# Kernel optimization log

Hardware: AMD Instinct MI355X
Metric: run time of the kernel (lower is better)

## Reference

```python
import jax, jax.numpy as jnp
import numpy as np

D_MODEL = 1024
N_HEADS = 16
D_KEYS = 64
D_LLM = 4096
B, L, S = 8, 1024, 1000
HD = N_HEADS * D_KEYS  # 1024


def setup_inputs() -> dict:
    key = jax.random.key(0)
    ks = jax.random.split(key, 12)
    sd = lambda fan_in: 1.0 / np.sqrt(fan_in)
    return {
        "target_embedding": jax.random.normal(ks[0], (B, L, D_MODEL), jnp.float32),
        "source_embedding": jax.random.normal(ks[1], (S, D_LLM), jnp.float32),
        "value_embedding": jax.random.normal(ks[2], (S, D_LLM), jnp.float32),
        "Wq": jax.random.normal(ks[3], (D_MODEL, HD), jnp.float32) * sd(D_MODEL),
        "bq": jnp.zeros((HD,), jnp.float32),
        "Wk": jax.random.normal(ks[4], (D_LLM, HD), jnp.float32) * sd(D_LLM),
        "bk": jnp.zeros((HD,), jnp.float32),
        "Wv": jax.random.normal(ks[5], (D_LLM, HD), jnp.float32) * sd(D_LLM),
        "bv": jnp.zeros((HD,), jnp.float32),
        "Wo": jax.random.normal(ks[6], (HD, D_LLM), jnp.float32) * sd(HD),
        "bo": jnp.zeros((D_LLM,), jnp.float32),
        "alpha": jnp.asarray(1.0, jnp.float32),
        "beta": jnp.asarray(0.5, jnp.float32),
    }


def reference(target_embedding, source_embedding, value_embedding,
              Wq, bq, Wk, bk, Wv, bv, Wo, bo, alpha, beta):
    # Projections
    q = (target_embedding @ Wq + bq).reshape(B, L, N_HEADS, D_KEYS)   # blhe
    k = (source_embedding @ Wk + bk).reshape(S, N_HEADS, D_KEYS)      # she
    v = (value_embedding @ Wv + bv).reshape(S, N_HEADS, D_KEYS)       # she
    # Reprogramming attention with alpha/beta scaling
    scale = 1.0 / np.sqrt(D_KEYS)
    scores = jnp.einsum('blhe,she->bhls', alpha * q, beta * k)        # BxHxLxS
    A = jax.nn.softmax(scale * scores, axis=-1)  # dropout is identity in eval
    out = jnp.einsum('bhls,she->blhe', A, v)
    out = out.reshape(B, L, HD)
    return out @ Wo + bo                                              # B,L,d_llm
```

## Files before the change

### kernel.cpp

```cpp
#include <hip/hip_runtime.h>

typedef unsigned short u16;
typedef __attribute__((ext_vector_type(8))) short short8;
typedef __attribute__((ext_vector_type(4))) float floatx4;

#define LOG2E 1.4426950408889634f

__device__ __forceinline__ u16 f2bf(float f) {
    unsigned u = __builtin_bit_cast(unsigned, f);
    u += 0x7fffu + ((u >> 16) & 1u);
    return (u16)(u >> 16);
}

__device__ __forceinline__ void gl2lds16(const void* g, void* l) {
    __builtin_amdgcn_global_load_lds((const __attribute__((address_space(1))) void*)g,
                                     (__attribute__((address_space(3))) void*)l,
                                     16, 0, 0);
}

__global__ __launch_bounds__(256) void conv_all(const float* __restrict__ T, u16* __restrict__ Tb,
                                                const float* __restrict__ Se, u16* __restrict__ Seb,
                                                const float* __restrict__ Ve, u16* __restrict__ Veb) {
    int g = blockIdx.x * 256 + threadIdx.x;
    const float* s; u16* d; int i; int nsrc;
    if (g < 2097152)      { s = T;  d = Tb;  i = g * 4;               nsrc = 8388608; }
    else if (g < 3145728) { s = Se; d = Seb; i = (g - 2097152) * 4;   nsrc = 4096000; }
    else                  { s = Ve; d = Veb; i = (g - 3145728) * 4;   nsrc = 4096000; }
    ushort4 o;
    if (i < nsrc) {
        float4 v = *(const float4*)(s + i);
        o.x = f2bf(v.x); o.y = f2bf(v.y); o.z = f2bf(v.z); o.w = f2bf(v.w);
    } else {
        o = make_ushort4(0, 0, 0, 0);
    }
    *(ushort4*)(d + i) = o;
}

__device__ __forceinline__ void transpose_core(const float* __restrict__ W, u16* __restrict__ Wt,
                                               int Kd, int Nd, int kx, int ny) {
    __shared__ u16 t[64][65];
    const int tid = threadIdx.x;
    const int k0 = kx * 64, n0 = ny * 64;
#pragma unroll
    for (int i = 0; i < 16; i++) {
        int r = i * 4 + (tid >> 6), c = tid & 63;
        t[r][c] = f2bf(W[(size_t)(k0 + r) * Nd + n0 + c]);
    }
    __syncthreads();
#pragma unroll
    for (int i = 0; i < 16; i++) {
        int n = i * 4 + (tid >> 6), k = tid & 63;
        Wt[(size_t)(n0 + n) * Kd + k0 + k] = t[k][n];
    }
}

__global__ __launch_bounds__(256) void transpose3(const float* __restrict__ Wq, u16* __restrict__ WqT,
                                                  const float* __restrict__ Wk, u16* __restrict__ WkT,
                                                  const float* __restrict__ Wv, u16* __restrict__ WvT) {
    int id = blockIdx.x;
    if (id < 256)       transpose_core(Wq, WqT, 1024, 1024, id & 15, id >> 4);
    else if (id < 1280) { int t = id - 256;  transpose_core(Wk, WkT, 4096, 1024, t & 63, t >> 6); }
    else                { int t = id - 1280; transpose_core(Wv, WvT, 4096, 1024, t & 63, t >> 6); }
}


__device__ __forceinline__
void stage_half(u16* dstA, u16* dstB, const u16* gA, const u16* gB, int Ks, int wave, int lane) {
    int r = lane >> 2;
    int cp = (lane & 3) * 8;
    const u16* a0 = gA + (size_t)(wave * 32 + r) * Ks + cp;
    const u16* b0 = gB + (size_t)(wave * 32 + r) * Ks + cp;
    const u16* a1 = gA + (size_t)(wave * 32 + 16 + r) * Ks + cp;
    const u16* b1 = gB + (size_t)(wave * 32 + 16 + r) * Ks + cp;
    gl2lds16(a0, dstA + wave * 1024);
    gl2lds16(b0, dstB + wave * 1024);
    gl2lds16(a1, dstA + wave * 1024 + 512);
    gl2lds16(b1, dstB + wave * 1024 + 512);
}

__device__ __forceinline__
void gemm8_core(const u16* __restrict__ A, const u16* __restrict__ Bt,
                const float* __restrict__ bias, void* __restrict__ Cout,
                int M, int N, int Ks, int Klen, int koff,
                int mode, float mult, int m0, int n0, u16* lds) {
    const int tid = threadIdx.x;
    const int wave = tid >> 6, lane = tid & 63;
    const int quad = lane >> 4, l16 = lane & 15;
    const int wm = wave >> 2, wn = wave & 3;

    floatx4 acc[8][4];
#pragma unroll
    for (int i = 0; i < 8; i++)
#pragma unroll
        for (int j = 0; j < 4; j++) acc[i][j] = (floatx4){0.f, 0.f, 0.f, 0.f};

    const u16* Ag = A + (size_t)m0 * Ks + koff;
    const u16* Bg = Bt + (size_t)n0 * Ks + koff;
    const int NT = Klen >> 6;

    const int raw = (wm * 128 + l16) * 32 + quad * 8;
    const int rbw = (wn * 64 + l16) * 32 + quad * 8;

    stage_half(lds, lds + 16384, Ag, Bg, Ks, wave, lane);
    stage_half(lds + 8192, lds + 24576, Ag + 32, Bg + 32, Ks, wave, lane);

#pragma unroll 1
    for (int t = 0; t < NT; ++t) {
        u16* cur = lds + (t & 1) * 32768;
        u16* nxt = lds + ((t + 1) & 1) * 32768;
        const u16* An = Ag + (size_t)(t + 1) * 64;
        const u16* Bn = Bg + (size_t)(t + 1) * 64;
        const bool st = (t + 1 < NT);
        short8 af[4], bf[4];

        asm volatile("s_waitcnt vmcnt(4)" ::: "memory");
        __builtin_amdgcn_sched_barrier(0);
        __builtin_amdgcn_s_barrier();
#pragma unroll
        for (int i = 0; i < 4; i++) af[i] = *(const short8*)&cur[raw + i * 512];
#pragma unroll
        for (int j = 0; j < 4; j++) bf[j] = *(const short8*)&cur[16384 + rbw + j * 512];
        if (st) stage_half(nxt, nxt + 16384, An, Bn, Ks, wave, lane);
        __builtin_amdgcn_s_setprio(1);
#pragma unroll
        for (int i = 0; i < 4; i++)
#pragma unroll
            for (int j = 0; j < 4; j++)
                acc[i][j] = __builtin_amdgcn_mfma_f32_16x16x32_bf16(af[i], bf[j], acc[i][j], 0, 0, 0);
        __builtin_amdgcn_s_setprio(0);

        __builtin_amdgcn_s_barrier();
#pragma unroll
        for (int i = 0; i < 4; i++) af[i] = *(const short8*)&cur[raw + 2048 + i * 512];
        __builtin_amdgcn_s_setprio(1);
#pragma unroll
        for (int i = 0; i < 4; i++)
#pragma unroll
            for (int j = 0; j < 4; j++)
                acc[i + 4][j] = __builtin_amdgcn_mfma_f32_16x16x32_bf16(af[i], bf[j], acc[i + 4][j], 0, 0, 0);
        __builtin_amdgcn_s_setprio(0);

        if (st) { asm volatile("s_waitcnt vmcnt(4)" ::: "memory"); }
        else    { asm volatile("s_waitcnt vmcnt(0)" ::: "memory"); }
        __builtin_amdgcn_sched_barrier(0);
        __builtin_amdgcn_s_barrier();
#pragma unroll
        for (int i = 0; i < 4; i++) af[i] = *(const short8*)&cur[8192 + raw + i * 512];
#pragma unroll
        for (int j = 0; j < 4; j++) bf[j] = *(const short8*)&cur[24576 + rbw + j * 512];
        if (st) stage_half(nxt + 8192, nxt + 24576, An + 32, Bn + 32, Ks, wave, lane);
        __builtin_amdgcn_s_setprio(1);
#pragma unroll
        for (int i = 0; i < 4; i++)
#pragma unroll
            for (int j = 0; j < 4; j++)
                acc[i][j] = __builtin_amdgcn_mfma_f32_16x16x32_bf16(af[i], bf[j], acc[i][j], 0, 0, 0);
        __builtin_amdgcn_s_setprio(0);

        __builtin_amdgcn_s_barrier();
#pragma unroll
        for (int i = 0; i < 4; i++) af[i] = *(const short8*)&cur[8192 + raw + 2048 + i * 512];
        __builtin_amdgcn_s_setprio(1);
#pragma unroll
        for (int i = 0; i < 4; i++)
#pragma unroll
            for (int j = 0; j < 4; j++)
                acc[i + 4][j] = __builtin_amdgcn_mfma_f32_16x16x32_bf16(af[i], bf[j], acc[i + 4][j], 0, 0, 0);
        __builtin_amdgcn_s_setprio(0);
    }

#pragma unroll
    for (int i = 0; i < 8; i++) {
#pragma unroll
        for (int j = 0; j < 4; j++) {
            int col = n0 + wn * 64 + j * 16 + l16;
            float bvv = (mode >= 4) ? 0.0f : bias[col];
#pragma unroll
            for (int r = 0; r < 4; r++) {
                int row = m0 + wm * 128 + i * 16 + quad * 4 + r;
                float v = (acc[i][j][r] + bvv) * mult;
                if (mode == 3 || mode == 4) {
                    ((float*)Cout)[(size_t)row * N + col] = v;
                } else if (mode == 5) {
                    ((float*)Cout)[(size_t)col * M + row] = v;
                } else {
                    ((u16*)Cout)[(size_t)row * N + col] = f2bf(v);
                }
            }
        }
    }
}

__global__ __launch_bounds__(512, 2)
void gemm_qkv(const u16* __restrict__ Tb, const u16* __restrict__ WqT, const float* __restrict__ bq,
              const u16* __restrict__ Seb, const u16* __restrict__ WkT,
              const u16* __restrict__ Veb, const u16* __restrict__ WvT,
              u16* __restrict__ Qb, float* __restrict__ KP, float* __restrict__ VPT,
              const float* __restrict__ alphaP, const float* __restrict__ betaP) {
    __shared__ u16 lds[65536];
    int b0 = blockIdx.x;
    int w = (b0 & 7) * 32 + (b0 >> 3);
    if (w < 128) {
        float mult = alphaP[0] * betaP[0] * 0.125f * LOG2E;
        gemm8_core(Tb, WqT, bq, Qb, 8192, 1024, 1024, 1024, 0,
                   1, mult, (w >> 2) * 256, (w & 3) * 256, lds);
    } else if (w < 192) {
        int t = w - 128; int kc = t >> 4;
        gemm8_core(Seb, WkT, nullptr, KP + (size_t)kc * 1048576, 1024, 1024, 4096, 1024, kc * 1024,
                   4, 1.0f, ((t >> 2) & 3) * 256, (t & 3) * 256, lds);
    } else {
        int t = w - 192; int kc = t >> 4;
        gemm8_core(Veb, WvT, nullptr, VPT + (size_t)kc * 1048576, 1024, 1024, 4096, 1024, kc * 1024,
                   5, 1.0f, ((t >> 2) & 3) * 256, (t & 3) * 256, lds);
    }
}

__global__ __launch_bounds__(512, 2)
void gemm_final(const u16* __restrict__ A, const u16* __restrict__ Bt,
                const float* __restrict__ bias, float* __restrict__ Cout) {
    __shared__ u16 lds[65536];
    int b0 = blockIdx.x;
    int idx = b0 >> 3;
    int m = (b0 & 7) * 4 + (idx >> 4);
    int n = idx & 15;
    gemm8_core(A, Bt, bias, Cout, 8192, 4096, 1024, 1024, 0, 3, 1.0f, m * 256, n * 256, lds);
}

__global__ __launch_bounds__(256)
void reduce_wo(const float* __restrict__ KP, const float* __restrict__ bk, u16* __restrict__ Kb,
               const float* __restrict__ VPT, const float* __restrict__ bv, u16* __restrict__ VTb,
               const float* __restrict__ Wo, u16* __restrict__ WoT) {
    int id = blockIdx.x;
    if (id >= 2048) {
        int t = id - 2048;
        transpose_core(Wo, WoT, 1024, 4096, t & 15, t >> 4);
        return;
    }
    const int tid = threadIdx.x;
    if (id < 1024) {
        int r = id, c = tid * 4;
        size_t base = (size_t)r * 1024 + c;
        float4 a0 = *(const float4*)(KP + base);
        float4 a1 = *(const float4*)(KP + 1048576 + base);
        float4 a2 = *(const float4*)(KP + 2097152 + base);
        float4 a3 = *(const float4*)(KP + 3145728 + base);
        float4 bb = *(const float4*)(bk + c);
        ushort4 o;
        o.x = f2bf(a0.x + a1.x + a2.x + a3.x + bb.x);
        o.y = f2bf(a0.y + a1.y + a2.y + a3.y + bb.y);
        o.z = f2bf(a0.z + a1.z + a2.z + a3.z + bb.z);
        o.w = f2bf(a0.w + a1.w + a2.w + a3.w + bb.w);
        *(ushort4*)(Kb + base) = o;
    } else {
        int d = id - 1024, s = tid * 4;
        size_t base = (size_t)d * 1024 + s;
        float4 a0 = *(const float4*)(VPT + base);
        float4 a1 = *(const float4*)(VPT + 1048576 + base);
        float4 a2 = *(const float4*)(VPT + 2097152 + base);
        float4 a3 = *(const float4*)(VPT + 3145728 + base);
        float bvv = bv[d];
        ushort4 o;
        o.x = f2bf(a0.x + a1.x + a2.x + a3.x + bvv);
        o.y = f2bf(a0.y + a1.y + a2.y + a3.y + bvv);
        o.z = f2bf(a0.z + a1.z + a2.z + a3.z + bvv);
        o.w = f2bf(a0.w + a1.w + a2.w + a3.w + bvv);
        *(ushort4*)(VTb + base) = o;
    }
}

__global__ __launch_bounds__(256, 2)
void attn_kernel(const u16* __restrict__ Q, const u16* __restrict__ Kb,
                 const u16* __restrict__ VT, u16* __restrict__ O) {
    __shared__ u16 sK[128 * 64];
    __shared__ u16 sV[64 * 128];
    __shared__ u16 sP[128 * 128];
    const int tid = threadIdx.x;
    const int wave = tid >> 6, lane = tid & 63;
    const int quad = lane >> 4, l16 = lane & 15;
    const int l7 = l16 & 7;
    const int bid = blockIdx.x;
    const int qt = bid & 7, h = (bid >> 3) & 15, b = bid >> 7;

    const u16* Qbase = Q + ((size_t)(b * 1024 + qt * 128 + wave * 32)) * 1024 + h * 64;
    short8 qf[2][2];
#pragma unroll
    for (int i = 0; i < 2; i++)
#pragma unroll
        for (int kk = 0; kk < 2; kk++)
            qf[i][kk] = *(const short8*)&Qbase[(size_t)(i * 16 + l16) * 1024 + kk * 32 + quad * 8];

    float psum[2] = {0.f, 0.f};
    floatx4 oacc[2][4];
#pragma unroll
    for (int i = 0; i < 2; i++)
#pragma unroll
        for (int n = 0; n < 4; n++) oacc[i][n] = (floatx4){0.f, 0.f, 0.f, 0.f};

    for (int st = 0; st < 8; ++st) {
#pragma unroll
        for (int i = 0; i < 4; i++) {
            int r = i * 32 + wave * 8 + (lane >> 3);
            int c = ((lane & 7) ^ ((lane >> 3) & 7)) * 8;
            gl2lds16(Kb + (size_t)(st * 128 + r) * 1024 + h * 64 + c, sK + i * 2048 + wave * 512);
        }
#pragma unroll
        for (int i = 0; i < 4; i++) {
            int r = i * 16 + wave * 4 + (lane >> 4);
            int c = ((lane & 15) ^ ((wave * 4 + (lane >> 4)) & 7)) * 8;
            gl2lds16(VT + (size_t)(h * 64 + r) * 1024 + st * 128 + c, sV + i * 2048 + wave * 512);
        }
        __syncthreads();

        floatx4 sacc[2][8];
#pragma unroll
        for (int i = 0; i < 2; i++)
#pragma unroll
            for (int j = 0; j < 8; j++) sacc[i][j] = (floatx4){0.f, 0.f, 0.f, 0.f};
#pragma unroll
        for (int kk = 0; kk < 2; kk++) {
            short8 kf[8];
#pragma unroll
            for (int j = 0; j < 8; j++)
                kf[j] = *(const short8*)&sK[(j * 16 + l16) * 64 + (((kk * 4 + quad) ^ l7) * 8)];
#pragma unroll
            for (int i = 0; i < 2; i++)
#pragma unroll
                for (int j = 0; j < 8; j++)
                    sacc[i][j] = __builtin_amdgcn_mfma_f32_16x16x32_bf16(kf[j], qf[i][kk], sacc[i][j], 0, 0, 0);
        }

#pragma unroll
        for (int i = 0; i < 2; i++) {
            const int rowbase = (wave * 32 + i * 16 + l16) * 128;
#pragma unroll
            for (int j = 0; j < 8; j++) {
                float p0 = exp2f(sacc[i][j][0]);
                float p1 = exp2f(sacc[i][j][1]);
                float p2 = exp2f(sacc[i][j][2]);
                float p3 = exp2f(sacc[i][j][3]);
                if (st == 7) {
                    if (j == 7 || (j == 6 && quad >= 2)) { p0 = p1 = p2 = p3 = 0.f; }
                }
                psum[i] += (p0 + p1) + (p2 + p3);
                uint2 val;
                val.x = (unsigned)f2bf(p0) | ((unsigned)f2bf(p1) << 16);
                val.y = (unsigned)f2bf(p2) | ((unsigned)f2bf(p3) << 16);
                int chunk = (2 * j + (quad >> 1)) ^ l7;
                *(uint2*)&sP[rowbase + chunk * 8 + (quad & 1) * 4] = val;
            }
        }

#pragma unroll
        for (int c = 0; c < 4; c++) {
            short8 pf[2], vf[4];
#pragma unroll
            for (int i = 0; i < 2; i++)
                pf[i] = *(const short8*)&sP[(wave * 32 + i * 16 + l16) * 128 + (((c * 4 + quad) ^ l7) * 8)];
#pragma unroll
            for (int n = 0; n < 4; n++)
                vf[n] = *(const short8*)&sV[(n * 16 + l16) * 128 + (((c * 4 + quad) ^ l7) * 8)];
#pragma unroll
            for (int i = 0; i < 2; i++)
#pragma unroll
                for (int n = 0; n < 4; n++)
                    oacc[i][n] = __builtin_amdgcn_mfma_f32_16x16x32_bf16(pf[i], vf[n], oacc[i][n], 0, 0, 0);
        }
        __syncthreads();
    }

#pragma unroll
    for (int i = 0; i < 2; i++) {
        psum[i] += __shfl_xor(psum[i], 16);
        psum[i] += __shfl_xor(psum[i], 32);
    }

    u16* Obase = O + ((size_t)(b * 1024 + qt * 128 + wave * 32)) * 1024 + h * 64;
#pragma unroll
    for (int i = 0; i < 2; i++) {
#pragma unroll
        for (int r = 0; r < 4; r++) {
            float l = __shfl(psum[i], (lane & 48) | (quad * 4 + r));
            float linv = 1.0f / l;
#pragma unroll
            for (int n = 0; n < 4; n++)
                Obase[(size_t)(i * 16 + quad * 4 + r) * 1024 + n * 16 + l16] = f2bf(oacc[i][n][r] * linv);
        }
    }
}

extern "C" void kernel_launch(void* const* d_in, const int* in_sizes, int n_in,
                              void* d_out, int out_size, void* d_ws, size_t ws_size,
                              hipStream_t stream) {
    const float* T     = (const float*)d_in[0];
    const float* Se    = (const float*)d_in[1];
    const float* Ve    = (const float*)d_in[2];
    const float* Wq    = (const float*)d_in[3];
    const float* bq    = (const float*)d_in[4];
    const float* Wk    = (const float*)d_in[5];
    const float* bk    = (const float*)d_in[6];
    const float* Wv    = (const float*)d_in[7];
    const float* bv    = (const float*)d_in[8];
    const float* Wo    = (const float*)d_in[9];
    const float* bo    = (const float*)d_in[10];
    const float* alpha = (const float*)d_in[11];
    const float* beta  = (const float*)d_in[12];

    char* ws = (char*)d_ws;
    size_t off = 0;
    auto alloc = [&](size_t bytes) { size_t o = off; off += (bytes + 255) & ~(size_t)255; return o; };

    u16* Tb  = (u16*)(ws + alloc((size_t)8192 * 1024 * 2));
    u16* Seb = (u16*)(ws + alloc((size_t)1024 * 4096 * 2));
    u16* Veb = (u16*)(ws + alloc((size_t)1024 * 4096 * 2));
    u16* WqT = (u16*)(ws + alloc((size_t)1024 * 1024 * 2));
    u16* WkT = (u16*)(ws + alloc((size_t)1024 * 4096 * 2));
    u16* WvT = (u16*)(ws + alloc((size_t)1024 * 4096 * 2));
    u16* Qb  = (u16*)(ws + alloc((size_t)8192 * 1024 * 2));
    u16* Kb  = (u16*)(ws + alloc((size_t)1024 * 1024 * 2));
    u16* VTb = (u16*)(ws + alloc((size_t)1024 * 1024 * 2));
    float* KP  = (float*)(ws + alloc((size_t)4 * 1024 * 1024 * 4));
    float* VPT = (float*)(ws + alloc((size_t)4 * 1024 * 1024 * 4));
    u16* Ob  = Tb;
    u16* WoT = Veb;

    conv_all<<<16384, 256, 0, stream>>>(T, Tb, Se, Seb, Ve, Veb);
    transpose3<<<2304, 256, 0, stream>>>(Wq, WqT, Wk, WkT, Wv, WvT);
    gemm_qkv<<<256, 512, 0, stream>>>(Tb, WqT, bq, Seb, WkT, Veb, WvT,
                                      Qb, KP, VPT, alpha, beta);
    reduce_wo<<<3072, 256, 0, stream>>>(KP, bk, Kb, VPT, bv, VTb, Wo, WoT);
    attn_kernel<<<1024, 256, 0, stream>>>(Qb, Kb, VTb, Ob);
    gemm_final<<<512, 512, 0, stream>>>(Ob, WoT, bo, (float*)d_out);
}
```

Before: 433.1 us.

## Swizzle GEMM LDS tiles and restage full K-tiles with double buffering

The shared GEMM core now stores each 64-wide K tile as full 64-element rows with an XOR swizzle on the 16-byte column chunks, so fragment reads from shared memory hit fewer bank conflicts. Staging moves from two half-tiles per iteration to one full tile loaded two iterations ahead into the buffer just consumed, with a single wait and barrier per iteration. The aim is to cut LDS bank conflicts and barrier/waitcnt overhead in the projection GEMMs. It adds an extra barrier before restaging and relies on the swizzle staying consistent between the global-to-LDS copy and the fragment reads.

```diff
diff --git a/kernel.cpp b/kernel.cpp
--- a/kernel.cpp
+++ b/kernel.cpp
@@ -64,18 +64,19 @@
 }
 
 
+__device__ __forceinline__ short8 ldsfrag(const u16* b, int row, int kk, int quad, int l7) {
+    return *(const short8*)&b[row * 64 + (((kk * 4 + quad) ^ l7) * 8)];
+}
+
 __device__ __forceinline__
-void stage_half(u16* dstA, u16* dstB, const u16* gA, const u16* gB, int Ks, int wave, int lane) {
-    int r = lane >> 2;
-    int cp = (lane & 3) * 8;
-    const u16* a0 = gA + (size_t)(wave * 32 + r) * Ks + cp;
-    const u16* b0 = gB + (size_t)(wave * 32 + r) * Ks + cp;
-    const u16* a1 = gA + (size_t)(wave * 32 + 16 + r) * Ks + cp;
-    const u16* b1 = gB + (size_t)(wave * 32 + 16 + r) * Ks + cp;
-    gl2lds16(a0, dstA + wave * 1024);
-    gl2lds16(b0, dstB + wave * 1024);
-    gl2lds16(a1, dstA + wave * 1024 + 512);
-    gl2lds16(b1, dstB + wave * 1024 + 512);
+void stage_tile(u16* dA, u16* dB, const u16* gA, const u16* gB, int Ks, int wave, int lane) {
+    int rl = wave * 8 + (lane >> 3);
+    int cs = ((lane & 7) ^ (rl & 7)) * 8;
+#pragma unroll
+    for (int ii = 0; ii < 4; ii++) {
+        gl2lds16(gA + (size_t)(ii * 64 + rl) * Ks + cs, dA + ii * 4096 + wave * 512);
+        gl2lds16(gB + (size_t)(ii * 64 + rl) * Ks + cs, dB + ii * 4096 + wave * 512);
+    }
 }
 
 __device__ __forceinline__
@@ -85,7 +86,7 @@
                 int mode, float mult, int m0, int n0, u16* lds) {
     const int tid = threadIdx.x;
     const int wave = tid >> 6, lane = tid & 63;
-    const int quad = lane >> 4, l16 = lane & 15;
+    const int quad = lane >> 4, l16 = lane & 15, l7 = l16 & 7;
     const int wm = wave >> 2, wn = wave & 3;
 
     floatx4 acc[8][4];
@@ -98,29 +99,29 @@
     const u16* Bg = Bt + (size_t)n0 * Ks + koff;
     const int NT = Klen >> 6;
 
-    const int raw = (wm * 128 + l16) * 32 + quad * 8;
-    const int rbw = (wn * 64 + l16) * 32 + quad * 8;
-
-    stage_half(lds, lds + 16384, Ag, Bg, Ks, wave, lane);
-    stage_half(lds + 8192, lds + 24576, Ag + 32, Bg + 32, Ks, wave, lane);
+    const int ra = wm * 128 + l16;
+    const int rb = wn * 64 + l16;
+
+    u16* A0 = lds;          u16* B0 = lds + 16384;
+    u16* A1 = lds + 32768;  u16* B1 = lds + 49152;
+
+    stage_tile(A0, B0, Ag, Bg, Ks, wave, lane);
+    stage_tile(A1, B1, Ag + 64, Bg + 64, Ks, wave, lane);
+    asm volatile("s_waitcnt vmcnt(8)" ::: "memory");
+    __builtin_amdgcn_sched_barrier(0);
+    __builtin_amdgcn_s_barrier();
+    __builtin_amdgcn_sched_barrier(0);
 
 #pragma unroll 1
     for (int t = 0; t < NT; ++t) {
-        u16* cur = lds + (t & 1) * 32768;
-        u16* nxt = lds + ((t + 1) & 1) * 32768;
-        const u16* An = Ag + (size_t)(t + 1) * 64;
-        const u16* Bn = Bg + (size_t)(t + 1) * 64;
-        const bool st = (t + 1 < NT);
+        u16* cA = (t & 1) ? A1 : A0;
+        u16* cB = (t & 1) ? B1 : B0;
         short8 af[4], bf[4];
 
-        asm volatile("s_waitcnt vmcnt(4)" ::: "memory");
-        __builtin_amdgcn_sched_barrier(0);
-        __builtin_amdgcn_s_barrier();
-#pragma unroll
-        for (int i = 0; i < 4; i++) af[i] = *(const short8*)&cur[raw + i * 512];
-#pragma unroll
-        for (int j = 0; j < 4; j++) bf[j] = *(const short8*)&cur[16384 + rbw + j * 512];
-        if (st) stage_half(nxt, nxt + 16384, An, Bn, Ks, wave, lane);
+#pragma unroll
+        for (int i = 0; i < 4; i++) af[i] = ldsfrag(cA, ra + i * 16, 0, quad, l7);
+#pragma unroll
+        for (int j = 0; j < 4; j++) bf[j] = ldsfrag(cB, rb + j * 16, 0, quad, l7);
         __builtin_amdgcn_s_setprio(1);
 #pragma unroll
         for (int i = 0; i < 4; i++)
@@ -128,10 +129,10 @@
             for (int j = 0; j < 4; j++)
                 acc[i][j] = __builtin_amdgcn_mfma_f32_16x16x32_bf16(af[i], bf[j], acc[i][j], 0, 0, 0);
         __builtin_amdgcn_s_setprio(0);
-
         __builtin_amdgcn_s_barrier();
-#pragma unroll
-        for (int i = 0; i < 4; i++) af[i] = *(const short8*)&cur[raw + 2048 + i * 512];
+
+#pragma unroll
+        for (int i = 0; i < 4; i++) af[i] = ldsfrag(cA, ra + 64 + i * 16, 0, quad, l7);
         __builtin_amdgcn_s_setprio(1);
 #pragma unroll
         for (int i = 0; i < 4; i++)
@@ -139,16 +140,12 @@
             for (int j = 0; j < 4; j++)
                 acc[i + 4][j] = __builtin_amdgcn_mfma_f32_16x16x32_bf16(af[i], bf[j], acc[i + 4][j], 0, 0, 0);
         __builtin_amdgcn_s_setprio(0);
-
-        if (st) { asm volatile("s_waitcnt vmcnt(4)" ::: "memory"); }
-        else    { asm volatile("s_waitcnt vmcnt(0)" ::: "memory"); }
-        __builtin_amdgcn_sched_barrier(0);
         __builtin_amdgcn_s_barrier();
-#pragma unroll
-        for (int i = 0; i < 4; i++) af[i] = *(const short8*)&cur[8192 + raw + i * 512];
-#pragma unroll
-        for (int j = 0; j < 4; j++) bf[j] = *(const short8*)&cur[24576 + rbw + j * 512];
-        if (st) stage_half(nxt + 8192, nxt + 24576, An + 32, Bn + 32, Ks, wave, lane);
+
+#pragma unroll
+        for (int i = 0; i < 4; i++) af[i] = ldsfrag(cA, ra + i * 16, 1, quad, l7);
+#pragma unroll
+        for (int j = 0; j < 4; j++) bf[j] = ldsfrag(cB, rb + j * 16, 1, quad, l7);
         __builtin_amdgcn_s_setprio(1);
 #pragma unroll
         for (int i = 0; i < 4; i++)
@@ -156,10 +153,10 @@
             for (int j = 0; j < 4; j++)
                 acc[i][j] = __builtin_amdgcn_mfma_f32_16x16x32_bf16(af[i], bf[j], acc[i][j], 0, 0, 0);
         __builtin_amdgcn_s_setprio(0);
-
         __builtin_amdgcn_s_barrier();
-#pragma unroll
-        for (int i = 0; i < 4; i++) af[i] = *(const short8*)&cur[8192 + raw + 2048 + i * 512];
+
+#pragma unroll
+        for (int i = 0; i < 4; i++) af[i] = ldsfrag(cA, ra + 64 + i * 16, 1, quad, l7);
         __builtin_amdgcn_s_setprio(1);
 #pragma unroll
         for (int i = 0; i < 4; i++)
@@ -167,6 +164,20 @@
             for (int j = 0; j < 4; j++)
                 acc[i + 4][j] = __builtin_amdgcn_mfma_f32_16x16x32_bf16(af[i], bf[j], acc[i + 4][j], 0, 0, 0);
         __builtin_amdgcn_s_setprio(0);
+        __builtin_amdgcn_s_barrier();
+
+        if (t + 2 < NT) {
+            stage_tile(cA, cB, Ag + (size_t)(t + 2) * 64, Bg + (size_t)(t + 2) * 64, Ks, wave, lane);
+            asm volatile("s_waitcnt vmcnt(8)" ::: "memory");
+            __builtin_amdgcn_sched_barrier(0);
+            __builtin_amdgcn_s_barrier();
+            __builtin_amdgcn_sched_barrier(0);
+        } else if (t + 1 < NT) {
+            asm volatile("s_waitcnt vmcnt(0)" ::: "memory");
+            __builtin_amdgcn_sched_barrier(0);
+            __builtin_amdgcn_s_barrier();
+            __builtin_amdgcn_sched_barrier(0);
+        }
     }
 
 #pragma unroll
```

New measurement: 431.2 us. About the same (-0.4%).
